# Performance work log

Hardware: AMD Instinct MI355X
Metric: run time of the kernel (lower is better)

Reference implementation:

```python
import jax, jax.numpy as jnp
import numpy as np

N = 200000
E = 3200000
EPS = 1e-5


def setup_inputs() -> dict:
    key = jax.random.key(0)
    ks = jax.random.split(key, 8)
    x = jax.random.normal(ks[0], (N, 128), dtype=jnp.float32)
    edge_index = jax.random.randint(ks[1], (2, E), 0, N, dtype=jnp.int32)
    def lin(k, fi, fo):
        s = 1.0 / np.sqrt(fi)
        return jax.random.uniform(k, (fi, fo), jnp.float32, -s, s)
    return {
        "x": x,
        "edge_index": edge_index,
        "W1": lin(ks[2], 128, 256), "b1": jnp.zeros((256,), jnp.float32),
        "gamma1": jnp.ones((256,), jnp.float32), "beta1": jnp.zeros((256,), jnp.float32),
        "W2": lin(ks[3], 256, 256), "b2": jnp.zeros((256,), jnp.float32),
        "gamma2": jnp.ones((256,), jnp.float32), "beta2": jnp.zeros((256,), jnp.float32),
        "W3": lin(ks[4], 256, 40), "b3": jnp.zeros((40,), jnp.float32),
    }


def _gcn_norm(edge_index):
    # add self-loops, compute symmetric GCN normalization
    loop = jnp.arange(N, dtype=jnp.int32)
    row = jnp.concatenate([edge_index[0], loop])
    col = jnp.concatenate([edge_index[1], loop])
    deg = jax.ops.segment_sum(jnp.ones_like(row, dtype=jnp.float32), row, num_segments=N)
    dinv = jax.lax.rsqrt(jnp.maximum(deg, 1.0))  # deg >= 1 due to self-loops
    norm = dinv[row] * dinv[col]  # [E+N]
    return row, col, norm


def _gcn_conv(x, W, b, row, col, norm):
    h = x @ W                                  # [N, Fout] small GEMM
    msg = h[col] * norm[:, None]               # gather + scale  [E+N, Fout]
    out = jax.ops.segment_sum(msg, row, num_segments=N)  # scatter-add
    return out + b


def _batchnorm(x, gamma, beta):
    mu = jnp.mean(x, axis=0)
    var = jnp.var(x, axis=0)
    return (x - mu) * jax.lax.rsqrt(var + EPS) * gamma + beta


def reference(x, edge_index, W1, b1, gamma1, beta1, W2, b2, gamma2, beta2, W3, b3):
    row, col, norm = _gcn_norm(edge_index)
    h = _gcn_conv(x, W1, b1, row, col, norm)
    h = jax.nn.relu(_batchnorm(h, gamma1, beta1))
    h = _gcn_conv(h, W2, b2, row, col, norm)
    h = jax.nn.relu(_batchnorm(h, gamma2, beta2))
    h = _gcn_conv(h, W3, b3, row, col, norm)
    return jax.nn.log_softmax(h, axis=-1)
```

## Files before the change

kernel.cpp:

```cpp
#include <hip/hip_runtime.h>
#include <hip/hip_bf16.h>

#define NNODES 200000
#define NEDGES 3200000
#define NBUCK 782
#define NEB 512
#define EPB (NEDGES / NEB)
#define EPS 1e-5f
#define AGGB_CHUNK 50000
#define AGGF_CHUNK 100000

typedef __bf16 bf16x8 __attribute__((ext_vector_type(8)));
typedef float  f32x4  __attribute__((ext_vector_type(4)));
typedef float  f32x2  __attribute__((ext_vector_type(2)));

__device__ __forceinline__ float bflo(unsigned u) { return __uint_as_float(u << 16); }
__device__ __forceinline__ float bfhi(unsigned u) { return __uint_as_float(u & 0xffff0000u); }
__device__ __forceinline__ unsigned short f2b(float f) {
    return __builtin_bit_cast(unsigned short, __float2bfloat16(f));
}
__device__ __forceinline__ unsigned pk2(float a, float b) {
    return (unsigned)f2b(a) | ((unsigned)f2b(b) << 16);
}
__device__ __forceinline__ unsigned bnrelu_pk(unsigned u, f32x2 c, f32x2 h) {
    f32x2 v = { __uint_as_float(u << 16), __uint_as_float(u & 0xffff0000u) };
    v = __builtin_elementwise_fma(v, c, h);
    const f32x2 z = {0.f, 0.f};
    v = __builtin_elementwise_max(v, z);
    return pk2(v[0], v[1]);
}

__device__ __forceinline__ void prepw_one(const float* __restrict__ W,
                                          unsigned short* __restrict__ Wswz,
                                          int K, int NOUT, int t) {
    int KSTEPS = K / 32;
    int lane = t & 63;
    int ks = (t >> 6) % KSTEPS;
    int g  = (t >> 6) / KSTEPS;
    int c = lane & 15, q = lane >> 4;
    int col = g * 16 + c;
    int k0 = ks * 32 + q * 8;
    unsigned short vals[8];
#pragma unroll
    for (int j = 0; j < 8; ++j)
        vals[j] = (col < NOUT) ? f2b(W[(size_t)(k0 + j) * NOUT + col]) : (unsigned short)0;
    *(uint4*)((char*)Wswz + (size_t)t * 16) = __builtin_bit_cast(uint4, vals);
}

__global__ __launch_bounds__(256) void k_cnt(const int* __restrict__ row, int* __restrict__ cnt,
                                             const float* __restrict__ W1,
                                             const float* __restrict__ W2,
                                             const float* __restrict__ W3,
                                             unsigned short* __restrict__ w1s,
                                             unsigned short* __restrict__ w2s,
                                             unsigned short* __restrict__ w3s,
                                             unsigned* __restrict__ statsz) {
    const int blk = blockIdx.x;
    if (blk == NEB + 56) {
        for (int i = threadIdx.x; i < 1026; i += 256) statsz[i] = 0u;
        return;
    }
    if (blk >= NEB) {
        int t = (blk - NEB) * 256 + threadIdx.x;
        if (t < 4096) prepw_one(W1, w1s, 128, 256, t);
        else if (t < 12288) prepw_one(W2, w2s, 256, 256, t - 4096);
        else if (t < 14336) prepw_one(W3, w3s, 256, 40, t - 12288);
        return;
    }
    __shared__ int h[NBUCK];
    for (int i = threadIdx.x; i < NBUCK; i += 256) h[i] = 0;
    __syncthreads();
    const int e0 = blk * EPB;
    for (int i = e0 + threadIdx.x; i < e0 + EPB; i += 256)
        atomicAdd(&h[row[i] >> 8], 1);
    __syncthreads();
    for (int i = threadIdx.x; i < NBUCK; i += 256)
        cnt[(size_t)blk * NBUCK + i] = h[i];
}

__global__ __launch_bounds__(256) void k_bscan(int* __restrict__ cnt, int* __restrict__ btot) {
    const int wv = (blockIdx.x * 256 + threadIdx.x) >> 6;
    const int lane = threadIdx.x & 63;
    if (wv >= NBUCK) return;
    int v[8]; int s = 0;
#pragma unroll
    for (int j = 0; j < 8; ++j) {
        v[j] = cnt[(size_t)(lane * 8 + j) * NBUCK + wv];
        s += v[j];
    }
    int excl = s;
#pragma unroll
    for (int o = 1; o < 64; o <<= 1) {
        int t = __shfl_up(excl, o);
        if (lane >= o) excl += t;
    }
    excl -= s;
    if (lane == 63) btot[wv] = excl + s;
    int base = excl;
#pragma unroll
    for (int j = 0; j < 8; ++j) {
        int t = v[j];
        cnt[(size_t)(lane * 8 + j) * NBUCK + wv] = base;
        base += t;
    }
}

__global__ __launch_bounds__(256) void k_place(const int* __restrict__ row, const int* __restrict__ col,
                                               const int* __restrict__ cnt, const int* __restrict__ btot,
                                               int* __restrict__ bbase, unsigned* __restrict__ ebuf) {
    __shared__ int sbb[NBUCK];
    __shared__ int tp[256];
    __shared__ int base[NBUCK];
    const int t = threadIdx.x;
    int v[4]; int loc = 0;
    const int i0 = t * 4;
#pragma unroll
    for (int j = 0; j < 4; ++j) {
        int idx = i0 + j;
        v[j] = (idx < NBUCK) ? btot[idx] : 0;
        loc += v[j];
    }
    tp[t] = loc;
    __syncthreads();
    for (int off = 1; off < 256; off <<= 1) {
        int u = (t >= off) ? tp[t - off] : 0;
        __syncthreads();
        tp[t] += u;
        __syncthreads();
    }
    int run = tp[t] - loc;
#pragma unroll
    for (int j = 0; j < 4; ++j) {
        int idx = i0 + j;
        if (idx < NBUCK) sbb[idx] = run;
        run += v[j];
    }
    __syncthreads();
    if (blockIdx.x == 0) {
        for (int i = t; i < NBUCK; i += 256) bbase[i] = sbb[i];
        if (t == 0) bbase[NBUCK] = NEDGES;
    }
    for (int i = t; i < NBUCK; i += 256)
        base[i] = sbb[i] + cnt[(size_t)blockIdx.x * NBUCK + i];
    __syncthreads();
    const int e0 = blockIdx.x * EPB;
    for (int i = e0 + t; i < e0 + EPB; i += 256) {
        int r = row[i], c = col[i];
        int p = atomicAdd(&base[r >> 8], 1);
        ebuf[p] = ((unsigned)(r & 255) << 18) | (unsigned)c;
    }
}

__global__ __launch_bounds__(256) void k_sort2(const unsigned* __restrict__ ebuf,
                                               const int* __restrict__ bbase,
                                               int* __restrict__ offs, float* __restrict__ dinv,
                                               int* __restrict__ csr,
                                               const float* __restrict__ x,
                                               uint4* __restrict__ xb) {
    __shared__ int cnt[256];
    __shared__ int sofs[256];
    __shared__ int sc[256];
    __shared__ float sdinv[256];
    const int b = blockIdx.x;
    const int t = threadIdx.x;
    const int n0 = b * 256;
    cnt[t] = 0;
    __syncthreads();
    const int s = bbase[b], e = bbase[b + 1];
    for (int i = s + t; i < e; i += 256)
        atomicAdd(&cnt[ebuf[i] >> 18], 1);
    __syncthreads();
    const int c = cnt[t];
    sc[t] = c;
    __syncthreads();
    for (int off = 1; off < 256; off <<= 1) {
        int v = (t >= off) ? sc[t - off] : 0;
        __syncthreads();
        sc[t] += v;
        __syncthreads();
    }
    const int excl = sc[t] - c;
    sofs[t] = s + excl;
    const int n = n0 + t;
    float dv = rsqrtf((float)(c + 1));
    sdinv[t] = dv;
    if (n < NNODES) {
        offs[n] = s + excl;
        dinv[n] = dv;
    }
    if (b == NBUCK - 1 && t == 0) offs[NNODES] = NEDGES;
    cnt[t] = 0;
    __syncthreads();
    for (int i = s + t; i < e; i += 256) {
        unsigned v = ebuf[i];
        int nl = v >> 18;
        int rank = atomicAdd(&cnt[nl], 1);
        csr[sofs[nl] + rank] = (int)(v & 0x3FFFFu);
    }
    const int nn = (NNODES - n0 < 256) ? (NNODES - n0) : 256;
    const float4* xp = (const float4*)(x + (size_t)n0 * 128);
    uint4* xo = xb + (size_t)n0 * 16;
    const int lim = nn * 16;
    for (int i = t; i < lim; i += 256) {
        float d = sdinv[i >> 4];
        float4 a = xp[i * 2], bb = xp[i * 2 + 1];
        uint4 o;
        o.x = pk2(a.x * d, a.y * d);  o.y = pk2(a.z * d, a.w * d);
        o.z = pk2(bb.x * d, bb.y * d); o.w = pk2(bb.z * d, bb.w * d);
        xo[i] = o;
    }
}

__global__ __launch_bounds__(256) void k_aggf(const uint4* __restrict__ in,
                                              const int* __restrict__ offs,
                                              const int* __restrict__ csr,
                                              const float* __restrict__ dinv,
                                              uint4* __restrict__ out,
                                              int nbase) {
    const int lane = threadIdx.x & 63;
    const int grp = lane >> 4;
    const int fl = lane & 15;
    const int node = nbase + blockIdx.x * 4 + (threadIdx.x >> 6);
    const int p0 = offs[node];
    const int K = offs[node + 1] - p0 + 1;
    float a0=0,a1=0,a2=0,a3=0,a4=0,a5=0,a6=0,a7=0;
    auto accum = [&](uint4 u) {
        a0 += bflo(u.x); a1 += bfhi(u.x);
        a2 += bflo(u.y); a3 += bfhi(u.y);
        a4 += bflo(u.z); a5 += bfhi(u.z);
        a6 += bflo(u.w); a7 += bfhi(u.w);
    };
    int k = 0;
    for (; k + 16 <= K; k += 16) {
        int j0 = k + grp;
        int i0 = (j0 == 0) ? node : csr[p0 + j0 - 1];
        int i1 = csr[p0 + k + 3 + grp];
        int i2 = csr[p0 + k + 7 + grp];
        int i3 = csr[p0 + k + 11 + grp];
        uint4 u0 = in[(size_t)i0 * 16 + fl];
        uint4 u1 = in[(size_t)i1 * 16 + fl];
        uint4 u2 = in[(size_t)i2 * 16 + fl];
        uint4 u3 = in[(size_t)i3 * 16 + fl];
        accum(u0); accum(u1); accum(u2); accum(u3);
    }
    for (; k + 8 <= K; k += 8) {
        int j0 = k + grp;
        int i0 = (j0 == 0) ? node : csr[p0 + j0 - 1];
        int i1 = csr[p0 + k + 3 + grp];
        uint4 u0 = in[(size_t)i0 * 16 + fl];
        uint4 u1 = in[(size_t)i1 * 16 + fl];
        accum(u0); accum(u1);
    }
    for (; k + 4 <= K; k += 4) {
        int j0 = k + grp;
        int i0 = (j0 == 0) ? node : csr[p0 + j0 - 1];
        accum(in[(size_t)i0 * 16 + fl]);
    }
    int rem = K - k;
    if (grp < rem) {
        int j0 = k + grp;
        int i0 = (j0 == 0) ? node : csr[p0 + j0 - 1];
        accum(in[(size_t)i0 * 16 + fl]);
    }
#define RED(v) v += __shfl_xor(v, 32); v += __shfl_xor(v, 16);
    RED(a0) RED(a1) RED(a2) RED(a3) RED(a4) RED(a5) RED(a6) RED(a7)
#undef RED
    if (grp == 0) {
        const float d = dinv[node];
        uint4 o;
        o.x = pk2(a0 * d, a1 * d); o.y = pk2(a2 * d, a3 * d);
        o.z = pk2(a4 * d, a5 * d); o.w = pk2(a6 * d, a7 * d);
        out[(size_t)node * 16 + fl] = o;
    }
}

__global__ __launch_bounds__(256) void k_aggb(const uint4* __restrict__ in,
                                              const int* __restrict__ offs,
                                              const int* __restrict__ csr,
                                              const float* __restrict__ dinv,
                                              uint4* __restrict__ out,
                                              int nbase) {
    const int lane = threadIdx.x & 63;
    const int half = lane >> 5;
    const int fl = lane & 31;
    const int node = nbase + blockIdx.x * 4 + (threadIdx.x >> 6);
    const int p0 = offs[node];
    const int K = offs[node + 1] - p0 + 1;
    float a0=0,a1=0,a2=0,a3=0,a4=0,a5=0,a6=0,a7=0;
    auto accum = [&](uint4 u) {
        a0 += bflo(u.x); a1 += bfhi(u.x);
        a2 += bflo(u.y); a3 += bfhi(u.y);
        a4 += bflo(u.z); a5 += bfhi(u.z);
        a6 += bflo(u.w); a7 += bfhi(u.w);
    };
    auto idxAt = [&](int j) -> int { return (j == 0) ? node : csr[p0 + j - 1]; };
    int k = 0;
    for (; k + 8 <= K; k += 8) {
        int i0 = idxAt(k + half);
        int i1 = csr[p0 + k + 1 + half];
        int i2 = csr[p0 + k + 3 + half];
        int i3 = csr[p0 + k + 5 + half];
        uint4 u0 = in[(size_t)i0 * 32 + fl];
        uint4 u1 = in[(size_t)i1 * 32 + fl];
        uint4 u2 = in[(size_t)i2 * 32 + fl];
        uint4 u3 = in[(size_t)i3 * 32 + fl];
        accum(u0); accum(u1); accum(u2); accum(u3);
    }
    for (; k + 2 <= K; k += 2) {
        accum(in[(size_t)idxAt(k + half) * 32 + fl]);
    }
    if (k < K && half == 0) {
        accum(in[(size_t)idxAt(k) * 32 + fl]);
    }
#define RED(v) v += __shfl_xor(v, 32);
    RED(a0) RED(a1) RED(a2) RED(a3) RED(a4) RED(a5) RED(a6) RED(a7)
#undef RED
    if (half == 0) {
        const float d = dinv[node];
        uint4 o;
        o.x = pk2(a0 * d, a1 * d); o.y = pk2(a2 * d, a3 * d);
        o.z = pk2(a4 * d, a5 * d); o.w = pk2(a6 * d, a7 * d);
        out[(size_t)node * 32 + fl] = o;
    }
}

__global__ __launch_bounds__(256) void k_agg3(const uint4* __restrict__ T3b,
                                              const int* __restrict__ offs,
                                              const int* __restrict__ csr,
                                              const float* __restrict__ dinv,
                                              const float* __restrict__ b3,
                                              float* __restrict__ out) {
    const int lane = threadIdx.x & 63;
    const int grp = lane / 5;
    const int fl = lane - grp * 5;
    const bool act = grp < 12;
    const int node = blockIdx.x * 4 + (threadIdx.x >> 6);
    const int p0 = offs[node];
    const int K = offs[node + 1] - p0 + 1;
    float a0=0,a1=0,a2=0,a3=0,a4=0,a5=0,a6=0,a7=0;
    auto accum = [&](uint4 u) {
        a0 += bflo(u.x); a1 += bfhi(u.x);
        a2 += bflo(u.y); a3 += bfhi(u.y);
        a4 += bflo(u.z); a5 += bfhi(u.z);
        a6 += bflo(u.w); a7 += bfhi(u.w);
    };
    const char* Tb = (const char*)T3b;
    int k = 0;
    if (act) {
        for (; k + 12 <= K; k += 12) {
            int j = k + grp;
            int i0 = (j == 0) ? node : csr[p0 + j - 1];
            accum(*(const uint4*)(Tb + (size_t)i0 * 128 + fl * 16));
        }
        int rem = K - k;
        if (grp < rem) {
            int j = k + grp;
            int i0 = (j == 0) ? node : csr[p0 + j - 1];
            accum(*(const uint4*)(Tb + (size_t)i0 * 128 + fl * 16));
        }
    }
#define RED3(v) { float t = __shfl(v, lane + 30); v += t; t = __shfl(v, lane + 15); v += t; \
                  float u1 = __shfl(v, lane + 5); float u2 = __shfl(v, lane + 10); v += u1 + u2; }
    RED3(a0) RED3(a1) RED3(a2) RED3(a3) RED3(a4) RED3(a5) RED3(a6) RED3(a7)
#undef RED3
    const float d = dinv[node];
    float v[8];
    if (grp == 0) {
        const float4* bp = (const float4*)(b3 + fl * 8);
        float4 b01 = bp[0], b23 = bp[1];
        v[0] = a0 * d + b01.x; v[1] = a1 * d + b01.y;
        v[2] = a2 * d + b01.z; v[3] = a3 * d + b01.w;
        v[4] = a4 * d + b23.x; v[5] = a5 * d + b23.y;
        v[6] = a6 * d + b23.z; v[7] = a7 * d + b23.w;
    } else {
#pragma unroll
        for (int j = 0; j < 8; ++j) v[j] = -INFINITY;
    }
    float m = v[0];
#pragma unroll
    for (int j = 1; j < 8; ++j) m = fmaxf(m, v[j]);
    float mm = __shfl(m, 0);
#pragma unroll
    for (int l = 1; l < 5; ++l) mm = fmaxf(mm, __shfl(m, l));
    float e = 0.f;
    if (grp == 0) {
#pragma unroll
        for (int j = 0; j < 8; ++j) e += __expf(v[j] - mm);
    }
    float s = __shfl(e, 0);
#pragma unroll
    for (int l = 1; l < 5; ++l) s += __shfl(e, l);
    float ls = __logf(s);
    if (grp == 0) {
        float* op = out + (size_t)node * 40 + fl * 8;
        float4 o0 = {v[0] - mm - ls, v[1] - mm - ls, v[2] - mm - ls, v[3] - mm - ls};
        float4 o1 = {v[4] - mm - ls, v[5] - mm - ls, v[6] - mm - ls, v[7] - mm - ls};
        *(float4*)op = o0;
        *(float4*)(op + 4) = o1;
    }
}

template <int K, int WNB, bool PRESCALE, bool BNA, bool STATS>
__global__ __launch_bounds__(256) void k_gemm(const __hip_bfloat16* __restrict__ A,
                                              const __hip_bfloat16* __restrict__ Wswz,
                                              const float* __restrict__ dinvp,
                                              const float* __restrict__ bnsc,
                                              const float* __restrict__ bnsh,
                                              unsigned short* __restrict__ Cout,
                                              int M, int NOUT, int CS,
                                              float* __restrict__ sums,
                                              float* __restrict__ sq,
                                              const float* __restrict__ gamma,
                                              const float* __restrict__ beta,
                                              float* __restrict__ scale,
                                              float* __restrict__ shift,
                                              int* __restrict__ done) {
    constexpr int KSTEPS = K / 32;
    constexpr int LROW   = K + 8;
    constexpr int U4R    = K / 8;
    constexpr int NU     = K / 32;
    constexpr int RPU    = 256 / U4R;
    __shared__ __align__(16) unsigned short As[64 * LROW];

    const int t = threadIdx.x;
    const int lane = t & 63;
    const int wid  = t >> 6;
    const int wn = wid * (WNB * 16);
    const long rowBase = (long)blockIdx.x * 64;
    const int cl = lane & 15, q = lane >> 4;

    const int cst = t % U4R;
    const int r0l = t / U4R;
    f32x2 cp[4], hp[4];
    if constexpr (BNA) {
        const f32x2* cpp = (const f32x2*)(bnsc + cst * 8);
        const f32x2* hpp = (const f32x2*)(bnsh + cst * 8);
#pragma unroll
        for (int j = 0; j < 4; ++j) { cp[j] = cpp[j]; hp[j] = hpp[j]; }
    }
    uint4 stg[NU];
#pragma unroll
    for (int u = 0; u < NU; ++u) {
        int rl = r0l + u * RPU;
        stg[u] = *(const uint4*)((const char*)A + (size_t)(rowBase + rl) * (K * 2) + (size_t)cst * 16);
    }
#pragma unroll
    for (int u = 0; u < NU; ++u) {
        uint4 v = stg[u];
        if constexpr (BNA) {
            v.x = bnrelu_pk(v.x, cp[0], hp[0]);
            v.y = bnrelu_pk(v.y, cp[1], hp[1]);
            v.z = bnrelu_pk(v.z, cp[2], hp[2]);
            v.w = bnrelu_pk(v.w, cp[3], hp[3]);
        }
        int rl = r0l + u * RPU;
        *(uint4*)&As[rl * LROW + cst * 8] = v;
    }
    __syncthreads();

    const __hip_bfloat16* bptr[WNB];
#pragma unroll
    for (int nf = 0; nf < WNB; ++nf)
        bptr[nf] = Wswz + (size_t)(wn / 16 + nf) * KSTEPS * 512 + (size_t)lane * 8;

    f32x4 acc[4][WNB];
    const f32x4 z = {0.f, 0.f, 0.f, 0.f};
#pragma unroll
    for (int mf = 0; mf < 4; ++mf)
#pragma unroll
        for (int nf = 0; nf < WNB; ++nf) acc[mf][nf] = z;

#pragma unroll
    for (int ks = 0; ks < KSTEPS; ++ks) {
        bf16x8 a[4], b[WNB];
#pragma unroll
        for (int nf = 0; nf < WNB; ++nf)
            b[nf] = __builtin_bit_cast(bf16x8, *(const uint4*)(bptr[nf] + ks * 512));
#pragma unroll
        for (int mf = 0; mf < 4; ++mf)
            a[mf] = __builtin_bit_cast(bf16x8, *(const uint4*)&As[(mf * 16 + cl) * LROW + ks * 32 + q * 8]);
#pragma unroll
        for (int mf = 0; mf < 4; ++mf)
#pragma unroll
            for (int nf = 0; nf < WNB; ++nf)
                acc[mf][nf] = __builtin_amdgcn_mfma_f32_16x16x32_bf16(a[mf], b[nf], acc[mf][nf], 0, 0, 0);
    }

#pragma unroll
    for (int mf = 0; mf < 4; ++mf)
#pragma unroll
        for (int i = 0; i < 4; ++i) {
            long row = rowBase + mf * 16 + q * 4 + i;
            if (row >= M) continue;
            float dv = PRESCALE ? dinvp[row] : 1.0f;
#pragma unroll
            for (int nf = 0; nf < WNB; ++nf) {
                int col = wn + nf * 16 + cl;
                if (col < NOUT)
                    Cout[row * CS + col] = f2b(PRESCALE ? acc[mf][nf][i] * dv : acc[mf][nf][i]);
            }
        }

    if constexpr (STATS) {
#pragma unroll
        for (int nf = 0; nf < WNB; ++nf) {
            float s = 0.f, s2 = 0.f;
#pragma unroll
            for (int mf = 0; mf < 4; ++mf)
#pragma unroll
                for (int i = 0; i < 4; ++i) {
                    long row = rowBase + mf * 16 + q * 4 + i;
                    float v = (row < M) ? acc[mf][nf][i] : 0.f;
                    s += v; s2 += v * v;
                }
            s  += __shfl_xor(s, 16);  s  += __shfl_xor(s, 32);
            s2 += __shfl_xor(s2, 16); s2 += __shfl_xor(s2, 32);
            if (q == 0) {
                int col = wn + nf * 16 + cl;
                if (col < NOUT) {
                    atomicAdd(&sums[col], s);
                    atomicAdd(&sq[col], s2);
                }
            }
        }
        __syncthreads();
        __shared__ int lastf;
        if (threadIdx.x == 0) lastf = (atomicAdd(done, 1) == (int)gridDim.x - 1) ? 1 : 0;
        __syncthreads();
        if (lastf) {
            const int tt = threadIdx.x;
            float su = atomicAdd(&sums[tt], 0.0f);
            float qu = atomicAdd(&sq[tt], 0.0f);
            float mu = su * (1.0f / NNODES);
            float var = qu * (1.0f / NNODES) - mu * mu;
            if (var < 0.f) var = 0.f;
            float sc = gamma[tt] * rsqrtf(var + EPS);
            scale[tt] = sc;
            shift[tt] = beta[tt] - mu * sc;
        }
    }
}

__global__ __launch_bounds__(256) void k_stats(const uint4* __restrict__ Zu,
                                               float* __restrict__ sums, float* __restrict__ sq,
                                               const float* __restrict__ gamma,
                                               const float* __restrict__ beta,
                                               float* __restrict__ scale, float* __restrict__ shift,
                                               int* __restrict__ done) {
    __shared__ float reds[8][256];
    __shared__ float redq[8][256];
    const int t = threadIdx.x;
    const int cg = t & 31;
    const int rs = t >> 5;
    const long r0 = (long)blockIdx.x * 256 + (long)rs * 32;
    float s[8], q[8];
#pragma unroll
    for (int j = 0; j < 8; ++j) { s[j] = 0.f; q[j] = 0.f; }
    for (int i = 0; i < 32; ++i) {
        long r = r0 + i;
        if (r >= NNODES) break;
        uint4 u = Zu[r * 32 + cg];
        float v0 = bflo(u.x), v1 = bfhi(u.x), v2 = bflo(u.y), v3 = bfhi(u.y);
        float v4 = bflo(u.z), v5 = bfhi(u.z), v6 = bflo(u.w), v7 = bfhi(u.w);
        s[0] += v0; q[0] += v0 * v0;  s[1] += v1; q[1] += v1 * v1;
        s[2] += v2; q[2] += v2 * v2;  s[3] += v3; q[3] += v3 * v3;
        s[4] += v4; q[4] += v4 * v4;  s[5] += v5; q[5] += v5 * v5;
        s[6] += v6; q[6] += v6 * v6;  s[7] += v7; q[7] += v7 * v7;
    }
#pragma unroll
    for (int j = 0; j < 8; ++j) {
        reds[rs][cg * 8 + j] = s[j];
        redq[rs][cg * 8 + j] = q[j];
    }
    __syncthreads();
    float S = 0.f, Q = 0.f;
#pragma unroll
    for (int j = 0; j < 8; ++j) { S += reds[j][t]; Q += redq[j][t]; }
    atomicAdd(&sums[t], S);
    atomicAdd(&sq[t], Q);
    __syncthreads();
    __shared__ int lastf;
    if (t == 0) lastf = (atomicAdd(done, 1) == (int)gridDim.x - 1) ? 1 : 0;
    __syncthreads();
    if (lastf) {
        float su = atomicAdd(&sums[t], 0.0f);
        float qu = atomicAdd(&sq[t], 0.0f);
        float mu = su * (1.0f / NNODES);
        float var = qu * (1.0f / NNODES) - mu * mu;
        if (var < 0.f) var = 0.f;
        float sc = gamma[t] * rsqrtf(var + EPS);
        scale[t] = sc;
        shift[t] = beta[t] - mu * sc;
    }
}

extern "C" void kernel_launch(void* const* d_in, const int* in_sizes, int n_in,
                              void* d_out, int out_size, void* d_ws, size_t ws_size,
                              hipStream_t stream) {
    const float* x   = (const float*)d_in[0];
    const int*   ei  = (const int*)d_in[1];
    const float* W1  = (const float*)d_in[2];
    const float* g1  = (const float*)d_in[4];
    const float* be1 = (const float*)d_in[5];
    const float* W2  = (const float*)d_in[6];
    const float* g2  = (const float*)d_in[8];
    const float* be2 = (const float*)d_in[9];
    const float* W3  = (const float*)d_in[10];
    const float* b3  = (const float*)d_in[11];

    char* w = (char*)d_ws;
    size_t o = 0;
    auto alloc = [&](size_t b) { size_t r = o; o += (b + 255) & ~(size_t)255; return r; };
    int*   offs = (int*)(w + alloc((size_t)(NNODES + 1) * 4));
    float* dinv = (float*)(w + alloc((size_t)NNODES * 4));
    int*   cnt  = (int*)(w + alloc((size_t)NEB * NBUCK * 4));
    int*   btot = (int*)(w + alloc(NBUCK * 4));
    int*   bbase= (int*)(w + alloc((NBUCK + 1) * 4));
    unsigned* ebuf = (unsigned*)(w + alloc((size_t)NEDGES * 4));
    int*   csr  = (int*)(w + alloc((size_t)NEDGES * 4));
    float* stats = (float*)(w + alloc(4 * 256 * 4 + 32));
    float* bnp   = (float*)(w + alloc(4 * 256 * 4));
    unsigned short* w1s = (unsigned short*)(w + alloc(65536));
    unsigned short* w2s = (unsigned short*)(w + alloc(131072));
    unsigned short* w3s = (unsigned short*)(w + alloc(32768));
    __hip_bfloat16* xb   = (__hip_bfloat16*)(w + alloc((size_t)NNODES * 128 * 2));
    __hip_bfloat16* buf0 = (__hip_bfloat16*)(w + alloc((size_t)NNODES * 128 * 2));
    __hip_bfloat16* buf1 = (__hip_bfloat16*)(w + alloc((size_t)NNODES * 256 * 2));
    __hip_bfloat16* buf2 = (__hip_bfloat16*)(w + alloc((size_t)NNODES * 256 * 2));

    float* sums1 = stats;       float* sq1 = stats + 256;
    float* sums2 = stats + 512; float* sq2 = stats + 768;
    int*   done1 = (int*)(stats + 1024);
    int*   done2 = done1 + 1;
    float* scale1 = bnp;        float* shift1 = bnp + 256;
    float* scale2 = bnp + 512;  float* shift2 = bnp + 768;

    const int SB = (NNODES + 255) / 256;
    const int GB = NNODES / 64;

    k_cnt<<<NEB + 57, 256, 0, stream>>>(ei, cnt, W1, W2, W3, w1s, w2s, w3s, (unsigned*)stats);
    k_bscan<<<(NBUCK * 64 + 255) / 256, 256, 0, stream>>>(cnt, btot);
    k_place<<<NEB, 256, 0, stream>>>(ei, ei + NEDGES, cnt, btot, bbase, ebuf);
    k_sort2<<<NBUCK, 256, 0, stream>>>(ebuf, bbase, offs, dinv, csr, x, (uint4*)xb);

    for (int c = 0; c < 2; ++c)
        k_aggf<<<AGGF_CHUNK / 4, 256, 0, stream>>>((const uint4*)xb, offs, csr, dinv, (uint4*)buf0, c * AGGF_CHUNK);
    k_gemm<128, 4, false, false, true><<<GB, 256, 0, stream>>>(buf0, (const __hip_bfloat16*)w1s, nullptr, nullptr, nullptr, (unsigned short*)buf1, NNODES, 256, 256, sums1, sq1, g1, be1, scale1, shift1, done1);

    k_gemm<256, 4, true, true, false><<<GB, 256, 0, stream>>>(buf1, (const __hip_bfloat16*)w2s, dinv, scale1, shift1, (unsigned short*)buf2, NNODES, 256, 256, nullptr, nullptr, nullptr, nullptr, nullptr, nullptr, nullptr);
    for (int c = 0; c < 4; ++c)
        k_aggb<<<AGGB_CHUNK / 4, 256, 0, stream>>>((const uint4*)buf2, offs, csr, dinv, (uint4*)buf1, c * AGGB_CHUNK);
    k_stats<<<SB, 256, 0, stream>>>((const uint4*)buf1, sums2, sq2, g2, be2, scale2, shift2, done2);

    k_gemm<256, 1, true, true, false><<<GB, 256, 0, stream>>>(buf1, (const __hip_bfloat16*)w3s, dinv, scale2, shift2, (unsigned short*)buf0, NNODES, 40, 64, nullptr, nullptr, nullptr, nullptr, nullptr, nullptr, nullptr);
    k_agg3<<<NNODES / 4, 256, 0, stream>>>((const uint4*)buf0, offs, csr, dinv, b3, (float*)d_out);
}
```

Before: 1.010 ms.

## Stage GEMM outputs through LDS for coalesced stores and replicate BN stat accumulators

```diff
diff --git a/kernel.cpp b/kernel.cpp
--- a/kernel.cpp
+++ b/kernel.cpp
@@ -9,6 +9,7 @@
 #define EPS 1e-5f
 #define AGGB_CHUNK 50000
 #define AGGF_CHUNK 100000
+#define NREP 16
 
 typedef __bf16 bf16x8 __attribute__((ext_vector_type(8)));
 typedef float  f32x4  __attribute__((ext_vector_type(4)));
@@ -56,8 +57,10 @@
                                              unsigned short* __restrict__ w3s,
                                              unsigned* __restrict__ statsz) {
     const int blk = blockIdx.x;
-    if (blk == NEB + 56) {
-        for (int i = threadIdx.x; i < 1026; i += 256) statsz[i] = 0u;
+    if (blk >= NEB + 56) {
+        const int zid = blk - (NEB + 56);
+        for (int i = zid * 256 + threadIdx.x; i < 2 * NREP * 512 + 2; i += 8 * 256)
+            statsz[i] = 0u;
         return;
     }
     if (blk >= NEB) {
@@ -400,16 +403,15 @@
     }
 }
 
-template <int K, int WNB, bool PRESCALE, bool BNA, bool STATS>
+template <int K, int WNB, int CS, bool PRESCALE, bool BNA, bool STATS>
 __global__ __launch_bounds__(256) void k_gemm(const __hip_bfloat16* __restrict__ A,
                                               const __hip_bfloat16* __restrict__ Wswz,
                                               const float* __restrict__ dinvp,
                                               const float* __restrict__ bnsc,
                                               const float* __restrict__ bnsh,
                                               unsigned short* __restrict__ Cout,
-                                              int M, int NOUT, int CS,
-                                              float* __restrict__ sums,
-                                              float* __restrict__ sq,
+                                              int M, int NOUT,
+                                              float* __restrict__ statr,
                                               const float* __restrict__ gamma,
                                               const float* __restrict__ beta,
                                               float* __restrict__ scale,
@@ -420,7 +422,13 @@
     constexpr int U4R    = K / 8;
     constexpr int NU     = K / 32;
     constexpr int RPU    = 256 / U4R;
-    __shared__ __align__(16) unsigned short As[64 * LROW];
+    constexpr int LROWC  = CS + 16;
+    constexpr int ABYTES = 64 * LROW * 2;
+    constexpr int CBYTES = 64 * LROWC * 2;
+    constexpr int SBYTES = (ABYTES > CBYTES) ? ABYTES : CBYTES;
+    __shared__ __align__(16) char smem[SBYTES];
+    unsigned short* As = (unsigned short*)smem;
+    unsigned short* Ct = (unsigned short*)smem;
 
     const int t = threadIdx.x;
     const int lane = t & 63;
@@ -486,22 +494,30 @@
                 acc[mf][nf] = __builtin_amdgcn_mfma_f32_16x16x32_bf16(a[mf], b[nf], acc[mf][nf], 0, 0, 0);
     }
 
+    __syncthreads();
 #pragma unroll
     for (int mf = 0; mf < 4; ++mf)
 #pragma unroll
         for (int i = 0; i < 4; ++i) {
-            long row = rowBase + mf * 16 + q * 4 + i;
-            if (row >= M) continue;
-            float dv = PRESCALE ? dinvp[row] : 1.0f;
-#pragma unroll
-            for (int nf = 0; nf < WNB; ++nf) {
-                int col = wn + nf * 16 + cl;
-                if (col < NOUT)
-                    Cout[row * CS + col] = f2b(PRESCALE ? acc[mf][nf][i] * dv : acc[mf][nf][i]);
-            }
+            int row = mf * 16 + q * 4 + i;
+            float dv = PRESCALE ? dinvp[rowBase + row] : 1.0f;
+#pragma unroll
+            for (int nf = 0; nf < WNB; ++nf)
+                Ct[row * LROWC + wn + nf * 16 + cl] = f2b(PRESCALE ? acc[mf][nf][i] * dv : acc[mf][nf][i]);
         }
+    __syncthreads();
+    constexpr int U4C = CS / 8;
+    constexpr int NC  = 64 * U4C / 256;
+#pragma unroll
+    for (int u = 0; u < NC; ++u) {
+        int idx = u * 256 + t;
+        int row = idx / U4C, c = idx % U4C;
+        uint4 v = *(const uint4*)&Ct[row * LROWC + c * 8];
+        *(uint4*)&Cout[(rowBase + row) * CS + c * 8] = v;
+    }
 
     if constexpr (STATS) {
+        float* rb = statr + (size_t)(blockIdx.x & (NREP - 1)) * 512;
 #pragma unroll
         for (int nf = 0; nf < WNB; ++nf) {
             float s = 0.f, s2 = 0.f;
@@ -509,8 +525,7 @@
             for (int mf = 0; mf < 4; ++mf)
 #pragma unroll
                 for (int i = 0; i < 4; ++i) {
-                    long row = rowBase + mf * 16 + q * 4 + i;
-                    float v = (row < M) ? acc[mf][nf][i] : 0.f;
+                    float v = acc[mf][nf][i];
                     s += v; s2 += v * v;
                 }
             s  += __shfl_xor(s, 16);  s  += __shfl_xor(s, 32);
@@ -518,8 +533,8 @@
             if (q == 0) {
                 int col = wn + nf * 16 + cl;
                 if (col < NOUT) {
-                    atomicAdd(&sums[col], s);
-                    atomicAdd(&sq[col], s2);
+                    atomicAdd(&rb[col], s);
+                    atomicAdd(&rb[256 + col], s2);
                 }
             }
         }
@@ -529,8 +544,12 @@
         __syncthreads();
         if (lastf) {
             const int tt = threadIdx.x;
-            float su = atomicAdd(&sums[tt], 0.0f);
-            float qu = atomicAdd(&sq[tt], 0.0f);
+            float su = 0.f, qu = 0.f;
+#pragma unroll
+            for (int r = 0; r < NREP; ++r) {
+                su += atomicAdd(&statr[(size_t)r * 512 + tt], 0.0f);
+                qu += atomicAdd(&statr[(size_t)r * 512 + 256 + tt], 0.0f);
+            }
             float mu = su * (1.0f / NNODES);
             float var = qu * (1.0f / NNODES) - mu * mu;
             if (var < 0.f) var = 0.f;
@@ -542,7 +561,7 @@
 }
 
 __global__ __launch_bounds__(256) void k_stats(const uint4* __restrict__ Zu,
-                                               float* __restrict__ sums, float* __restrict__ sq,
+                                               float* __restrict__ statr,
                                                const float* __restrict__ gamma,
                                                const float* __restrict__ beta,
                                                float* __restrict__ scale, float* __restrict__ shift,
@@ -576,15 +595,20 @@
     float S = 0.f, Q = 0.f;
 #pragma unroll
     for (int j = 0; j < 8; ++j) { S += reds[j][t]; Q += redq[j][t]; }
-    atomicAdd(&sums[t], S);
-    atomicAdd(&sq[t], Q);
+    float* rb = statr + (size_t)(blockIdx.x & (NREP - 1)) * 512;
+    atomicAdd(&rb[t], S);
+    atomicAdd(&rb[256 + t], Q);
     __syncthreads();
     __shared__ int lastf;
     if (t == 0) lastf = (atomicAdd(done, 1) == (int)gridDim.x - 1) ? 1 : 0;
     __syncthreads();
     if (lastf) {
-        float su = atomicAdd(&sums[t], 0.0f);
-        float qu = atomicAdd(&sq[t], 0.0f);
+        float su = 0.f, qu = 0.f;
+#pragma unroll
+        for (int r = 0; r < NREP; ++r) {
+            su += atomicAdd(&statr[(size_t)r * 512 + t], 0.0f);
+            qu += atomicAdd(&statr[(size_t)r * 512 + 256 + t], 0.0f);
+        }
         float mu = su * (1.0f / NNODES);
         float var = qu * (1.0f / NNODES) - mu * mu;
         if (var < 0.f) var = 0.f;
@@ -618,7 +642,7 @@
     int*   bbase= (int*)(w + alloc((NBUCK + 1) * 4));
     unsigned* ebuf = (unsigned*)(w + alloc((size_t)NEDGES * 4));
     int*   csr  = (int*)(w + alloc((size_t)NEDGES * 4));
-    float* stats = (float*)(w + alloc(4 * 256 * 4 + 32));
+    float* stats = (float*)(w + alloc((2 * NREP * 512 + 8) * 4));
     float* bnp   = (float*)(w + alloc(4 * 256 * 4));
     unsigned short* w1s = (unsigned short*)(w + alloc(65536));
     unsigned short* w2s = (unsigned short*)(w + alloc(131072));
@@ -628,9 +652,9 @@
     __hip_bfloat16* buf1 = (__hip_bfloat16*)(w + alloc((size_t)NNODES * 256 * 2));
     __hip_bfloat16* buf2 = (__hip_bfloat16*)(w + alloc((size_t)NNODES * 256 * 2));
 
-    float* sums1 = stats;       float* sq1 = stats + 256;
-    float* sums2 = stats + 512; float* sq2 = stats + 768;
-    int*   done1 = (int*)(stats + 1024);
+    float* statr1 = stats;
+    float* statr2 = stats + NREP * 512;
+    int*   done1 = (int*)(stats + 2 * NREP * 512);
     int*   done2 = done1 + 1;
     float* scale1 = bnp;        float* shift1 = bnp + 256;
     float* scale2 = bnp + 512;  float* shift2 = bnp + 768;
@@ -638,20 +662,20 @@
     const int SB = (NNODES + 255) / 256;
     const int GB = NNODES / 64;
 
-    k_cnt<<<NEB + 57, 256, 0, stream>>>(ei, cnt, W1, W2, W3, w1s, w2s, w3s, (unsigned*)stats);
+    k_cnt<<<NEB + 64, 256, 0, stream>>>(ei, cnt, W1, W2, W3, w1s, w2s, w3s, (unsigned*)stats);
     k_bscan<<<(NBUCK * 64 + 255) / 256, 256, 0, stream>>>(cnt, btot);
     k_place<<<NEB, 256, 0, stream>>>(ei, ei + NEDGES, cnt, btot, bbase, ebuf);
     k_sort2<<<NBUCK, 256, 0, stream>>>(ebuf, bbase, offs, dinv, csr, x, (uint4*)xb);
 
     for (int c = 0; c < 2; ++c)
         k_aggf<<<AGGF_CHUNK / 4, 256, 0, stream>>>((const uint4*)xb, offs, csr, dinv, (uint4*)buf0, c * AGGF_CHUNK);
-    k_gemm<128, 4, false, false, true><<<GB, 256, 0, stream>>>(buf0, (const __hip_bfloat16*)w1s, nullptr, nullptr, nullptr, (unsigned short*)buf1, NNODES, 256, 256, sums1, sq1, g1, be1, scale1, shift1, done1);
-
-    k_gemm<256, 4, true, true, false><<<GB, 256, 0, stream>>>(buf1, (const __hip_bfloat16*)w2s, dinv, scale1, shift1, (unsigned short*)buf2, NNODES, 256, 256, nullptr, nullptr, nullptr, nullptr, nullptr, nullptr, nullptr);
+    k_gemm<128, 4, 256, false, false, true><<<GB, 256, 0, stream>>>(buf0, (const __hip_bfloat16*)w1s, nullptr, nullptr, nullptr, (unsigned short*)buf1, NNODES, 256, statr1, g1, be1, scale1, shift1, done1);
+
+    k_gemm<256, 4, 256, true, true, false><<<GB, 256, 0, stream>>>(buf1, (const __hip_bfloat16*)w2s, dinv, scale1, shift1, (unsigned short*)buf2, NNODES, 256, nullptr, nullptr, nullptr, nullptr, nullptr, nullptr);
     for (int c = 0; c < 4; ++c)
         k_aggb<<<AGGB_CHUNK / 4, 256, 0, stream>>>((const uint4*)buf2, offs, csr, dinv, (uint4*)buf1, c * AGGB_CHUNK);
-    k_stats<<<SB, 256, 0, stream>>>((const uint4*)buf1, sums2, sq2, g2, be2, scale2, shift2, done2);
-
-    k_gemm<256, 1, true, true, false><<<GB, 256, 0, stream>>>(buf1, (const __hip_bfloat16*)w3s, dinv, scale2, shift2, (unsigned short*)buf0, NNODES, 40, 64, nullptr, nullptr, nullptr, nullptr, nullptr, nullptr, nullptr);
+    k_stats<<<SB, 256, 0, stream>>>((const uint4*)buf1, statr2, g2, be2, scale2, shift2, done2);
+
+    k_gemm<256, 1, 64, true, true, false><<<GB, 256, 0, stream>>>(buf1, (const __hip_bfloat16*)w3s, dinv, scale2, shift2, (unsigned short*)buf0, NNODES, 40, nullptr, nullptr, nullptr, nullptr, nullptr, nullptr);
     k_agg3<<<NNODES / 4, 256, 0, stream>>>((const uint4*)buf0, offs, csr, dinv, b3, (float*)d_out);
 }
```

After: 937.4 us. 7.2% less time.
